# Performance work log

Hardware: AMD Instinct MI355X
Metric: run time of the kernel (lower is better)

Reference implementation:

```python
import jax, jax.numpy as jnp
import numpy as np
import math

D_MODEL = 1024
NUM_HEADS = 16


def setup_inputs() -> dict:
    key = jax.random.key(0)
    ks = jax.random.split(key, 5)
    B, S, D = 4, 2048, D_MODEL
    scale = 1.0 / math.sqrt(D)
    x = jax.random.normal(ks[0], (B, S, D), dtype=jnp.float32)
    wq = jax.random.normal(ks[1], (D, D), dtype=jnp.float32) * scale
    wk = jax.random.normal(ks[2], (D, D), dtype=jnp.float32) * scale
    wv = jax.random.normal(ks[3], (D, D), dtype=jnp.float32) * scale
    wo = jax.random.normal(ks[4], (D, D), dtype=jnp.float32) * scale
    return {"x": x, "wq": wq, "wk": wk, "wv": wv, "wo": wo}


def _mhsa(x, wq, wk, wv, wo):
    B, S, D = x.shape
    H = NUM_HEADS
    dk = D // H
    # projections: y = x @ W^T
    q = (x @ wq.T).reshape(B, S, H, dk).transpose(0, 2, 1, 3)  # [B,H,S,dk]
    k = (x @ wk.T).reshape(B, S, H, dk).transpose(0, 2, 1, 3)
    v = (x @ wv.T).reshape(B, S, H, dk).transpose(0, 2, 1, 3)
    scores = jnp.einsum("bhqd,bhkd->bhqk", q, k) / jnp.sqrt(jnp.asarray(dk, x.dtype))
    mask = jnp.tril(jnp.ones((S, S), dtype=bool))  # [S,S] causal
    neg_inf = jnp.asarray(-jnp.inf, scores.dtype)
    scores_masked = jnp.where(mask, scores, neg_inf)
    max_scores = jnp.max(scores_masked, axis=-1, keepdims=True)
    max_scores = jnp.where(jnp.isfinite(max_scores), max_scores, jnp.zeros_like(max_scores))
    exp_scores = jnp.exp(scores - max_scores) * mask.astype(scores.dtype)
    denom = jnp.maximum(exp_scores.sum(axis=-1, keepdims=True), 1e-9)
    attn = exp_scores / denom
    out = jnp.einsum("bhqk,bhkd->bhqd", attn, v)  # [B,H,S,dk]
    out = out.transpose(0, 2, 1, 3).reshape(B, S, D)
    return out @ wo.T


def reference(x, wq, wk, wv, wo):
    return _mhsa(x, wq, wk, wv, wo)
```

## Files before the change

kernel.cpp:

```cpp
#include <hip/hip_runtime.h>
#include <stdint.h>


typedef __attribute__((ext_vector_type(8))) short short8;
typedef __attribute__((ext_vector_type(4))) short short4v;
typedef __attribute__((ext_vector_type(4))) float float4v;
typedef __attribute__((ext_vector_type(2))) unsigned int uint2v;

#define QSCALE 0.18033688011112042f
#define EXP_C2 5.770780163555852f

__device__ inline short f2bf(float f) {
  union { float f; uint32_t u; } v; v.f = f;
  uint32_t r = (v.u + 0x7fffu + ((v.u >> 16) & 1)) >> 16;
  return (short)(uint16_t)r;
}

__device__ inline unsigned int pack2bf(float a, float b) {
  union { float f; unsigned int u; } ua, ub;
  ua.f = a; ub.f = b;
  return __builtin_amdgcn_perm(ub.u, ua.u, 0x07060302u);
}

__device__ inline void async_copy16(const void* g, void* l) {
  __builtin_amdgcn_global_load_lds(
      (const __attribute__((address_space(1))) void*)g,
      (__attribute__((address_space(3))) void*)l, 16, 0, 0);
}

__global__ __launch_bounds__(256) void cvtAll(
    const float* __restrict__ x, const float* __restrict__ wq,
    const float* __restrict__ wk, const float* __restrict__ wv,
    const float* __restrict__ wo,
    short* __restrict__ xb, short* __restrict__ wqb, short* __restrict__ wkb,
    short* __restrict__ wvb, short* __restrict__ wob) {
  const int b = blockIdx.x;
  const float* s; short* d; int base;
  if (b < 8192) { s = x; d = xb; base = b; }
  else {
    const int wi = (b - 8192) >> 10; base = (b - 8192) & 1023;
    s = (wi == 0) ? wq : (wi == 1) ? wk : (wi == 2) ? wv : wo;
    d = (wi == 0) ? wqb : (wi == 1) ? wkb : (wi == 2) ? wvb : wob;
  }
  const size_t i = (size_t)base * 256 + threadIdx.x;
  const float4v v = *(const float4v*)(s + 4 * i);
  short4v o;
  o[0] = f2bf(v[0]); o[1] = f2bf(v[1]);
  o[2] = f2bf(v[2]); o[3] = f2bf(v[3]);
  *(short4v*)(d + 4 * i) = o;
}

template <int MODE>
__global__ __launch_bounds__(256) void gemm_bt(
    const short* __restrict__ A,
    const short* __restrict__ W0, const short* __restrict__ W1,
    const short* __restrict__ W2,
    short* __restrict__ Yb0, short* __restrict__ Yb1, short* __restrict__ Yb2,
    float* __restrict__ Yf) {
  constexpr int Kd = 1024;
  __shared__ __align__(16) short As[128 * 32];
  __shared__ __align__(16) short Bs[128 * 32];

  const int t = threadIdx.x;
  const int w = t >> 6, l = t & 63, l15 = l & 15, quad = l >> 4;
  const int wm = w >> 1, wn = w & 1;

  int mblk, nblk, zz = 0;
  {
    const int o = blockIdx.x;
    const int xcd = o & 7, slot = o >> 3;
    mblk = (xcd << 3) | (slot & 7);
    const int c = slot >> 3;
    if (MODE == 0) { nblk = c & 7; zz = c >> 3; }
    else nblk = c;
  }
  const int m0 = mblk * 128, n0 = nblk * 128;

  const short* W = W0;
  short* Yb = Yb0;
  float sc = 1.0f;
  if (MODE == 0) {
    if (zz == 0) sc = QSCALE;
    else if (zz == 1) { W = W1; Yb = Yb1; }
    else { W = W2; Yb = Yb2; }
  }

  float4v acc[4][4];
#pragma unroll
  for (int i = 0; i < 4; i++)
#pragma unroll
    for (int j = 0; j < 4; j++) acc[i][j] = (float4v){0.f, 0.f, 0.f, 0.f};

  const int r4 = t >> 2, c48 = (t & 3) * 8;
  const short* Wbase = W + (n0 + r4) * Kd + c48;
  short* AsW = &As[w * 512];
  short* BsW = &Bs[w * 512];
  const int i0 = m0 + r4;
  const int i1 = m0 + 64 + r4;

  for (int k0 = 0; k0 < Kd; k0 += 32) {
    if (MODE == 0) {
      async_copy16(A + (size_t)i0 * Kd + k0 + c48, AsW);
      async_copy16(A + (size_t)i1 * Kd + k0 + c48, AsW + 2048);
    } else {
      const int k = k0 + c48, h = k >> 6, dd = k & 63;
      async_copy16(A + ((((size_t)(i0 >> 11) * 16 + h) * 2048 + (i0 & 2047)) * 64 + dd), AsW);
      async_copy16(A + ((((size_t)(i1 >> 11) * 16 + h) * 2048 + (i1 & 2047)) * 64 + dd), AsW + 2048);
    }
    async_copy16(Wbase + k0, BsW);
    async_copy16(Wbase + 64 * Kd + k0, BsW + 2048);
    __syncthreads();
    short8 af[4], bf[4];
#pragma unroll
    for (int mi = 0; mi < 4; mi++)
      af[mi] = *(const short8*)&As[(wm * 64 + mi * 16 + l15) * 32 + quad * 8];
#pragma unroll
    for (int ni = 0; ni < 4; ni++)
      bf[ni] = *(const short8*)&Bs[(wn * 64 + ni * 16 + l15) * 32 + quad * 8];
#pragma unroll
    for (int mi = 0; mi < 4; mi++)
#pragma unroll
      for (int ni = 0; ni < 4; ni++)
        acc[mi][ni] = __builtin_amdgcn_mfma_f32_16x16x32_bf16(
            af[mi], bf[ni], acc[mi][ni], 0, 0, 0);
    __syncthreads();
  }

#pragma unroll
  for (int mi = 0; mi < 4; mi++) {
    const int ib = m0 + wm * 64 + mi * 16 + quad * 4;
#pragma unroll
    for (int ni = 0; ni < 4; ni++) {
      const int j = n0 + wn * 64 + ni * 16 + l15;
#pragma unroll
      for (int r = 0; r < 4; r++) {
        const int i = ib + r;
        if (MODE == 0) {
          Yb[((((size_t)(i >> 11) * 16 + (j >> 6)) * 2048 + (i & 2047)) * 64 + (j & 63))] =
              f2bf(acc[mi][ni][r] * sc);
        } else {
          Yf[(size_t)i * 1024 + j] = acc[mi][ni][r];
        }
      }
    }
  }
}

__global__ __launch_bounds__(256) void transV(const short* __restrict__ V,
                                              short* __restrict__ VT) {
  __shared__ __align__(16) short Ls[64 * 72];
  const int t = threadIdx.x;
  const int s0 = blockIdx.x * 64, bh = blockIdx.y;
  const short* Vh = V + (size_t)bh * 2048 * 64;
  short* Th = VT + (size_t)bh * 64 * 2048;
  const int r = t >> 2, c = (t & 3) * 16;
  *(short8*)&Ls[r * 72 + c] = *(const short8*)&Vh[(size_t)(s0 + r) * 64 + c];
  *(short8*)&Ls[r * 72 + c + 8] = *(const short8*)&Vh[(size_t)(s0 + r) * 64 + c + 8];
  __syncthreads();
  short8 o0, o1;
#pragma unroll
  for (int j = 0; j < 8; j++) {
    o0[j] = Ls[(c + j) * 72 + r];
    o1[j] = Ls[(c + 8 + j) * 72 + r];
  }
  *(short8*)&Th[(size_t)r * 2048 + s0 + c] = o0;
  *(short8*)&Th[(size_t)r * 2048 + s0 + c + 8] = o1;
}

__global__ __launch_bounds__(256) void attn4(
    short* __restrict__ Q,
    const short* __restrict__ K,
    const short* __restrict__ VT) {
  __shared__ __align__(16) short Ks[2][64 * 64];
  __shared__ __align__(16) short Vs[2][64 * 64];
  __shared__ __align__(16) short Ps[4][16 * 64];

  const int t = threadIdx.x;
  const int w = t >> 6, l = t & 63, l15 = l & 15, quad = l >> 4;
  const int bh = blockIdx.x;
  const int qp = blockIdx.y;
  short* Qh = Q + (size_t)bh * 2048 * 64;
  const short* Kh = K + (size_t)bh * 2048 * 64;
  const short* Vh = VT + (size_t)bh * 64 * 2048;

  const int sr = t >> 2, c0 = t & 3;
  const int ssw = sr & 7;
  const int stA = sr * 64 + (((2 * c0) ^ ssw) << 3);
  const int stB = sr * 64 + (((2 * c0 + 1) ^ ssw) << 3);
  const int gA = c0 * 16, gB = c0 * 16 + 8;

  const int fsw = l15 & 7;
  const int fc0 = (quad ^ fsw) << 3;
  const int fc1 = ((4 + quad) ^ fsw) << 3;
  short* PsW = &Ps[w][0];
  const int pwr = l15 * 64;

  short8 ones;
#pragma unroll
  for (int j = 0; j < 8; j++) ones[j] = (short)0x3F80;
  const float4v initC = (float4v){-EXP_C2, -EXP_C2, -EXP_C2, -EXP_C2};

  for (int pass = 0; pass < 2; pass++) {
    const int q0 = (pass ? (31 - qp) : qp) * 64;
    const int qn = q0 + w * 16 + l15;
    const short8 qf0 = *(const short8*)&Qh[(size_t)qn * 64 + quad * 8];
    const short8 qf1 = *(const short8*)&Qh[(size_t)qn * 64 + 32 + quad * 8];

    float4v acc[4];
#pragma unroll
    for (int dt = 0; dt < 4; dt++) acc[dt] = (float4v){0.f, 0.f, 0.f, 0.f};
    float4v accL = (float4v){0.f, 0.f, 0.f, 0.f};

    short8 kv0 = *(const short8*)&Kh[(size_t)sr * 64 + gA];
    short8 kv1 = *(const short8*)&Kh[(size_t)sr * 64 + gB];
    short8 vv0 = *(const short8*)&Vh[(size_t)sr * 2048 + gA];
    short8 vv1 = *(const short8*)&Vh[(size_t)sr * 2048 + gB];

    int p = 0;
    for (int kb = 0; kb <= q0; kb += 64, p ^= 1) {
      const bool diag = (kb == q0);
      short* KsP = &Ks[p][0];
      short* VsP = &Vs[p][0];
      *(short8*)&KsP[stA] = kv0;
      *(short8*)&KsP[stB] = kv1;
      *(short8*)&VsP[stA] = vv0;
      *(short8*)&VsP[stB] = vv1;
      __syncthreads();

      const int kb2 = diag ? kb : kb + 64;
      kv0 = *(const short8*)&Kh[(size_t)(kb2 + sr) * 64 + gA];
      kv1 = *(const short8*)&Kh[(size_t)(kb2 + sr) * 64 + gB];
      vv0 = *(const short8*)&Vh[(size_t)sr * 2048 + kb2 + gA];
      vv1 = *(const short8*)&Vh[(size_t)sr * 2048 + kb2 + gB];

#pragma unroll
      for (int kt = 0; kt < 4; kt++) {
        const int krb = (kt * 16 + l15) * 64;
        const short8 kf0 = *(const short8*)&KsP[krb + fc0];
        const short8 kf1 = *(const short8*)&KsP[krb + fc1];
        __builtin_amdgcn_s_setprio(1);
        float4v s = __builtin_amdgcn_mfma_f32_16x16x32_bf16(kf0, qf0, initC, 0, 0, 0);
        s = __builtin_amdgcn_mfma_f32_16x16x32_bf16(kf1, qf1, s, 0, 0, 0);
        __builtin_amdgcn_s_setprio(0);
        float p0 = __builtin_amdgcn_exp2f(s[0]);
        float p1 = __builtin_amdgcn_exp2f(s[1]);
        float p2 = __builtin_amdgcn_exp2f(s[2]);
        float p3 = __builtin_amdgcn_exp2f(s[3]);
        if (diag) {
          const int key = kb + kt * 16 + quad * 4;
          p0 = (key <= qn) ? p0 : 0.f;
          p1 = (key + 1 <= qn) ? p1 : 0.f;
          p2 = (key + 2 <= qn) ? p2 : 0.f;
          p3 = (key + 3 <= qn) ? p3 : 0.f;
        }
        uint2v pw;
        pw[0] = pack2bf(p0, p1);
        pw[1] = pack2bf(p2, p3);
        *(uint2v*)&PsW[pwr + (((2 * kt + (quad >> 1)) ^ fsw) << 3) +
                       ((quad & 1) << 2)] = pw;
      }
      __builtin_amdgcn_wave_barrier();

      const short8 pf0 = *(const short8*)&PsW[pwr + fc0];
      const short8 pf1 = *(const short8*)&PsW[pwr + fc1];
      __builtin_amdgcn_s_setprio(1);
#pragma unroll
      for (int dt = 0; dt < 4; dt++) {
        const int vrb = (dt * 16 + l15) * 64;
        const short8 vf0 = *(const short8*)&VsP[vrb + fc0];
        const short8 vf1 = *(const short8*)&VsP[vrb + fc1];
        acc[dt] = __builtin_amdgcn_mfma_f32_16x16x32_bf16(vf0, pf0, acc[dt], 0, 0, 0);
        acc[dt] = __builtin_amdgcn_mfma_f32_16x16x32_bf16(vf1, pf1, acc[dt], 0, 0, 0);
      }
      accL = __builtin_amdgcn_mfma_f32_16x16x32_bf16(ones, pf0, accL, 0, 0, 0);
      accL = __builtin_amdgcn_mfma_f32_16x16x32_bf16(ones, pf1, accL, 0, 0, 0);
      __builtin_amdgcn_s_setprio(0);
    }

    const float inv = 1.0f / fmaxf(accL[0], 1e-30f);
#pragma unroll
    for (int dt = 0; dt < 4; dt++) {
      short4v o;
#pragma unroll
      for (int ri = 0; ri < 4; ri++) o[ri] = f2bf(acc[dt][ri] * inv);
      *(short4v*)&Qh[(size_t)qn * 64 + dt * 16 + quad * 4] = o;
    }
    if (pass == 0) __syncthreads();
  }
}

extern "C" void kernel_launch(void* const* d_in, const int* in_sizes, int n_in,
                              void* d_out, int out_size, void* d_ws,
                              size_t ws_size, hipStream_t stream) {
  const float* x = (const float*)d_in[0];
  const float* wq = (const float*)d_in[1];
  const float* wk = (const float*)d_in[2];
  const float* wv = (const float*)d_in[3];
  const float* wo = (const float*)d_in[4];
  float* out = (float*)d_out;

  short* xb = (short*)d_out;
  short* vtg = xb + (size_t)8192 * 1024;

  short* wqb = (short*)d_ws;
  short* wkb = wqb + (size_t)1024 * 1024;
  short* wvb = wkb + (size_t)1024 * 1024;
  short* wob = wvb + (size_t)1024 * 1024;
  short* qws = wob + (size_t)1024 * 1024;
  short* kws = qws + (size_t)8192 * 1024;
  short* vws = kws + (size_t)8192 * 1024;

  cvtAll<<<12288, 256, 0, stream>>>(x, wq, wk, wv, wo, xb, wqb, wkb, wvb, wob);
  gemm_bt<0><<<1536, 256, 0, stream>>>(
      xb, wqb, wkb, wvb, qws, kws, vws, nullptr);
  transV<<<dim3(32, 64), 256, 0, stream>>>(vws, vtg);
  attn4<<<dim3(64, 16), 256, 0, stream>>>(qws, kws, vtg);
  gemm_bt<1><<<512, 256, 0, stream>>>(
      qws, wob, nullptr, nullptr, nullptr, nullptr, nullptr, out);
}
```

Baseline: 245.0 us.

## Double-buffer LDS tiles in projection GEMM to overlap loads with MFMA

The A and B tiles in shared memory get two buffers each. The load of the next K-slice is issued before the MFMA work on the current slice, so global-to-LDS copies can overlap with compute instead of waiting at a barrier first. This doubles the GEMM's LDS footprint, which may lower occupancy. It also relies on the end-of-iteration barrier to drain the async copies.

```diff
diff --git a/kernel.cpp b/kernel.cpp
--- a/kernel.cpp
+++ b/kernel.cpp
@@ -58,8 +58,8 @@
     short* __restrict__ Yb0, short* __restrict__ Yb1, short* __restrict__ Yb2,
     float* __restrict__ Yf) {
   constexpr int Kd = 1024;
-  __shared__ __align__(16) short As[128 * 32];
-  __shared__ __align__(16) short Bs[128 * 32];
+  __shared__ __align__(16) short As[2][128 * 32];
+  __shared__ __align__(16) short Bs[2][128 * 32];
 
   const int t = threadIdx.x;
   const int w = t >> 6, l = t & 63, l15 = l & 15, quad = l >> 4;
@@ -93,30 +93,38 @@
 
   const int r4 = t >> 2, c48 = (t & 3) * 8;
   const short* Wbase = W + (n0 + r4) * Kd + c48;
-  short* AsW = &As[w * 512];
-  short* BsW = &Bs[w * 512];
+  const int ldsW = w * 512;
   const int i0 = m0 + r4;
   const int i1 = m0 + 64 + r4;
 
-  for (int k0 = 0; k0 < Kd; k0 += 32) {
+  auto STAGE = [&](int k0, int b) {
     if (MODE == 0) {
-      async_copy16(A + (size_t)i0 * Kd + k0 + c48, AsW);
-      async_copy16(A + (size_t)i1 * Kd + k0 + c48, AsW + 2048);
+      async_copy16(A + (size_t)i0 * Kd + k0 + c48, &As[b][ldsW]);
+      async_copy16(A + (size_t)i1 * Kd + k0 + c48, &As[b][ldsW + 2048]);
     } else {
       const int k = k0 + c48, h = k >> 6, dd = k & 63;
-      async_copy16(A + ((((size_t)(i0 >> 11) * 16 + h) * 2048 + (i0 & 2047)) * 64 + dd), AsW);
-      async_copy16(A + ((((size_t)(i1 >> 11) * 16 + h) * 2048 + (i1 & 2047)) * 64 + dd), AsW + 2048);
+      async_copy16(A + ((((size_t)(i0 >> 11) * 16 + h) * 2048 + (i0 & 2047)) * 64 + dd),
+                   &As[b][ldsW]);
+      async_copy16(A + ((((size_t)(i1 >> 11) * 16 + h) * 2048 + (i1 & 2047)) * 64 + dd),
+                   &As[b][ldsW + 2048]);
     }
-    async_copy16(Wbase + k0, BsW);
-    async_copy16(Wbase + 64 * Kd + k0, BsW + 2048);
-    __syncthreads();
+    async_copy16(Wbase + k0, &Bs[b][ldsW]);
+    async_copy16(Wbase + 64 * Kd + k0, &Bs[b][ldsW + 2048]);
+  };
+
+  STAGE(0, 0);
+  __syncthreads();
+
+  for (int k0 = 0; k0 < Kd; k0 += 32) {
+    const int cur = (k0 >> 5) & 1;
+    if (k0 + 32 < Kd) STAGE(k0 + 32, cur ^ 1);
     short8 af[4], bf[4];
 #pragma unroll
     for (int mi = 0; mi < 4; mi++)
-      af[mi] = *(const short8*)&As[(wm * 64 + mi * 16 + l15) * 32 + quad * 8];
+      af[mi] = *(const short8*)&As[cur][(wm * 64 + mi * 16 + l15) * 32 + quad * 8];
 #pragma unroll
     for (int ni = 0; ni < 4; ni++)
-      bf[ni] = *(const short8*)&Bs[(wn * 64 + ni * 16 + l15) * 32 + quad * 8];
+      bf[ni] = *(const short8*)&Bs[cur][(wn * 64 + ni * 16 + l15) * 32 + quad * 8];
 #pragma unroll
     for (int mi = 0; mi < 4; mi++)
 #pragma unroll
```

Result: no change. 243.0 us (median of 3 runs) (-0.8%).
